# Kernel tuning notes

Measured on AMD Instinct MI355X. Metric: run time of the kernel, lower is better.

The kernel has to match this reference:

```python
import jax, jax.numpy as jnp
import numpy as np
import math

B, L, D = 8, 2048, 256


def setup_inputs() -> dict:
    key = jax.random.key(0)
    ks = jax.random.split(key, 8)
    return {
        "query": jax.random.normal(ks[0], (B, L, D), dtype=jnp.float32),
        "key": jax.random.normal(ks[1], (B, L, D), dtype=jnp.float32),
        "value": jax.random.normal(ks[2], (B, L, D), dtype=jnp.float32),
        "mask": jax.random.randint(ks[3], (B, L), 0, 2, dtype=jnp.int32),
        "Wq_w": jax.random.normal(ks[4], (D, D), dtype=jnp.float32) * 0.05,
        "Wq_b": jax.random.normal(ks[5], (D,), dtype=jnp.float32) * 0.05,
        "Wk_w": jax.random.normal(ks[6], (D, D), dtype=jnp.float32) * 0.05,
        "Wk_b": jax.random.normal(ks[7], (D,), dtype=jnp.float32) * 0.05,
    }


def reference(query, key, value, mask, Wq_w, Wq_b, Wk_w, Wk_b):
    d = query.shape[-1]
    q = query @ Wq_w.T + Wq_b            # [B, Lq, D]
    k = key @ Wk_w.T + Wk_b              # [B, Lk, D]
    scores = jnp.einsum("bqd,bkd->bqk", q, k) / math.sqrt(d)  # [B, Lq, Lk]
    m = mask.astype(scores.dtype)[:, None, :]                  # [B, 1, Lk]
    # multiplicative then additive masking, as in original
    scores = jnp.where(m == 0, jnp.asarray(-1e9, scores.dtype), scores * m)
    attn = jax.nn.softmax(scores, axis=-1)
    return jnp.einsum("bqk,bkd->bqd", attn, value)
```

## Files before the change

kernel.cpp:

```cpp
#include <hip/hip_runtime.h>
#include <stdint.h>
#include <stddef.h>

#define B_ 8
#define L_ 2048
#define D_ 256
#define KSPLIT 4
#define KRANGE 512
#define KTILE 32
#define NITER 16

typedef __bf16 bf16x8 __attribute__((ext_vector_type(8)));
typedef float floatx4 __attribute__((ext_vector_type(4)));
typedef float floatx16 __attribute__((ext_vector_type(16)));
typedef _Float16 half4_t __attribute__((ext_vector_type(4)));

__device__ __forceinline__ short f2bf(float f) {
    union { float f; uint32_t u; } v; v.f = f;
    return (short)((v.u + 0x8000u) >> 16);
}

__device__ __forceinline__ uint32_t pack2bf(float a, float b) {
    union { float f; uint32_t u; } x, y; x.f = a; y.f = b;
    return ((x.u + 0x8000u) >> 16) | ((y.u + 0x8000u) & 0xFFFF0000u);
}

__device__ __forceinline__ uint32_t cvtpk_bf16(float lo, float hi2) {
    uint32_t w;
    asm("v_cvt_pk_bf16_f32 %0, %1, %2" : "=v"(w) : "v"(lo), "v"(hi2));
    return w;
}

__device__ __forceinline__ void pl32swap(uint32_t &a, uint32_t &b) {
    asm("v_permlane32_swap_b32 %0, %1" : "+v"(a), "+v"(b));
}

__device__ __forceinline__ void async16(const void* g, void* l) {
    __builtin_amdgcn_global_load_lds(
        (__attribute__((address_space(1))) void*)g,
        (__attribute__((address_space(3))) void*)l,
        16, 0, 0);
}

__global__ __launch_bounds__(256, 3) void proj_kernel(
    const float* __restrict__ Xq, const float* __restrict__ Xk,
    const float* __restrict__ Wq, const float* __restrict__ Wk,
    const float* __restrict__ bq, const float* __restrict__ bk,
    short* __restrict__ Oq, short* __restrict__ Ok)
{
    const float* X    = blockIdx.y ? Xk : Xq;
    const float* W    = blockIdx.y ? Wk : Wq;
    const float* bias = blockIdx.y ? bk : bq;
    short* Out        = blockIdx.y ? Ok : Oq;

    __shared__ uint32_t As[2][64 * 20];
    __shared__ uint32_t Ws[2][256 * 20];

    const int tid  = threadIdx.x;
    const int wid  = tid >> 6;
    const int lane = tid & 63;
    const int m16  = lane & 15;
    const int quad = lane >> 4;
    const int row0 = blockIdx.x * 64;
    const int ar = tid >> 2, cg = tid & 3;

    floatx4 acc[16];
    const floatx4 z4 = {0.f, 0.f, 0.f, 0.f};
#pragma unroll
    for (int i = 0; i < 16; i++) acc[i] = z4;

    {
        const float* srcA = X + (size_t)(row0 + ar) * D_ + cg * 8;
        float4 a = *(const float4*)srcA, b2 = *(const float4*)(srcA + 4);
        uint4 u; u.x = pack2bf(a.x, a.y); u.y = pack2bf(a.z, a.w);
        u.z = pack2bf(b2.x, b2.y); u.w = pack2bf(b2.z, b2.w);
        *(uint4*)&As[0][ar * 20 + cg * 4] = u;
#pragma unroll
        for (int p = 0; p < 4; p++) {
            const float* srcW = W + (size_t)(p * 64 + ar) * D_ + cg * 8;
            float4 wa = *(const float4*)srcW, wb = *(const float4*)(srcW + 4);
            uint4 w; w.x = pack2bf(wa.x, wa.y); w.y = pack2bf(wa.z, wa.w);
            w.z = pack2bf(wb.x, wb.y); w.w = pack2bf(wb.z, wb.w);
            *(uint4*)&Ws[0][(p * 64 + ar) * 20 + cg * 4] = w;
        }
    }
    __syncthreads();

    for (int kc = 0; kc < 8; kc++) {
        const int buf = kc & 1;
        float4 na, nb, nwa[4], nwb[4];
        if (kc < 7) {
            const int k1 = (kc + 1) * 32;
            const float* srcA = X + (size_t)(row0 + ar) * D_ + k1 + cg * 8;
            na = *(const float4*)srcA; nb = *(const float4*)(srcA + 4);
#pragma unroll
            for (int p = 0; p < 4; p++) {
                const float* srcW = W + (size_t)(p * 64 + ar) * D_ + k1 + cg * 8;
                nwa[p] = *(const float4*)srcW; nwb[p] = *(const float4*)(srcW + 4);
            }
        }
        bf16x8 af = *(const bf16x8*)&As[buf][(wid * 16 + m16) * 20 + quad * 4];
#pragma unroll
        for (int n = 0; n < 16; n++) {
            bf16x8 bfr = *(const bf16x8*)&Ws[buf][(n * 16 + m16) * 20 + quad * 4];
            acc[n] = __builtin_amdgcn_mfma_f32_16x16x32_bf16(af, bfr, acc[n], 0, 0, 0);
        }
        if (kc < 7) {
            uint4 u; u.x = pack2bf(na.x, na.y); u.y = pack2bf(na.z, na.w);
            u.z = pack2bf(nb.x, nb.y); u.w = pack2bf(nb.z, nb.w);
            *(uint4*)&As[buf ^ 1][ar * 20 + cg * 4] = u;
#pragma unroll
            for (int p = 0; p < 4; p++) {
                uint4 w; w.x = pack2bf(nwa[p].x, nwa[p].y); w.y = pack2bf(nwa[p].z, nwa[p].w);
                w.z = pack2bf(nwb[p].x, nwb[p].y); w.w = pack2bf(nwb[p].z, nwb[p].w);
                *(uint4*)&Ws[buf ^ 1][(p * 64 + ar) * 20 + cg * 4] = w;
            }
        }
        __syncthreads();
    }
#pragma unroll
    for (int n = 0; n < 16; n++) {
        const int col = n * 16 + m16;
        const float bv = bias[col];
#pragma unroll
        for (int r = 0; r < 4; r++) {
            const int row = row0 + wid * 16 + quad * 4 + r;
            Out[(size_t)row * D_ + col] = f2bf(acc[n][r] + bv);
        }
    }
}

__global__ __launch_bounds__(256, 2) void vtrans_kernel(
    const float* __restrict__ V, short* __restrict__ Vt)
{
    __shared__ uint32_t T[256 * 20];
    const int tid = threadIdx.x;
    const int b  = blockIdx.y;
    const int l0 = blockIdx.x * 32;
    const int r2 = tid >> 4;
    const int dg = tid & 15;
    const int lp = r2 ^ ((dg & 3) << 2);
#pragma unroll
    for (int p = 0; p < 4; p++) {
        int d0 = (dg + p * 16) * 4;
        const float* src = V + ((size_t)b * L_ + l0 + r2 * 2) * D_ + d0;
        float4 e0 = *(const float4*)src;
        float4 e1 = *(const float4*)(src + D_);
        T[(d0 + 0) * 20 + lp] = pack2bf(e0.x, e1.x);
        T[(d0 + 1) * 20 + lp] = pack2bf(e0.y, e1.y);
        T[(d0 + 2) * 20 + lp] = pack2bf(e0.z, e1.z);
        T[(d0 + 3) * 20 + lp] = pack2bf(e0.w, e1.w);
    }
    __syncthreads();
#pragma unroll
    for (int p = 0; p < 4; p++) {
        int d = (tid >> 2) + p * 64;
        int c = tid & 3;
        int cp = c ^ ((d >> 2) & 3);
        uint4 u = *(const uint4*)&T[d * 20 + cp * 4];
        *(uint4*)(Vt + ((size_t)b * D_ + d) * L_ + l0 + c * 8) = u;
    }
}

__global__ __launch_bounds__(256, 2) void flash_kernel(
    const short* __restrict__ Qb, const short* __restrict__ Kb,
    const short* __restrict__ Vt, const int* __restrict__ mask,
    float* __restrict__ Out, _Float16* __restrict__ Part,
    float* __restrict__ Lpart)
{
    __shared__ short Ks[2][KTILE * 256];
    __shared__ short Vs[2][256 * KTILE];

    const int tid  = threadIdx.x;
    const int wid  = tid >> 6;
    const int lane = tid & 63;
    const int l31  = lane & 31;
    const int hi   = lane >> 5;
    const int b  = blockIdx.x;
    const int q0 = blockIdx.y * 128;
    const int z  = blockIdx.z;

    const short* kbase = Kb + ((size_t)b * L_ + z * KRANGE) * D_;
    const short* vbase = Vt + (size_t)b * D_ * L_;
    const int*   mg    = mask + b * L_ + z * KRANGE;

    bf16x8 qf[16];
    {
        const short* qrow = Qb + ((size_t)b * L_ + q0 + wid * 32 + l31) * D_ + hi * 8;
#pragma unroll
        for (int dt = 0; dt < 16; dt++)
            qf[dt] = *(const bf16x8*)(qrow + dt * 16);
    }

    floatx16 o[8];
#pragma unroll
    for (int n = 0; n < 8; n++)
#pragma unroll
        for (int r = 0; r < 16; r++) o[n][r] = 0.f;
    float rsum = 0.f;

    auto stageK = [&](int t, int bufi) {
        short* kl = &Ks[bufi][0];
#pragma unroll
        for (int c = 0; c < 4; c++) {
            int unit = wid * 4 + c;
            int row = unit * 2 + (lane >> 5);
            int g = (lane & 31) ^ (row & 7);
            async16(kbase + (size_t)(t * KTILE + row) * D_ + g * 8, kl + unit * 512);
        }
    };
    auto stageV = [&](int t, int bufi) {
        short* vl = &Vs[bufi][0];
#pragma unroll
        for (int c = 0; c < 4; c++) {
            int unit = wid * 4 + c;
            int d = unit * 16 + (lane >> 2);
            int g = (lane & 3) ^ ((lane >> 2) & 3);
            async16(vbase + (size_t)d * L_ + z * KRANGE + t * KTILE + g * 8, vl + unit * 512);
        }
    };

    stageK(0, 0);
    __builtin_amdgcn_s_waitcnt(0x0F70);
    __syncthreads();

    const float C2 = 0.09016844f;
    bf16x8 pfA, pfB;

    for (int t = 0; t < NITER; t++) {
        const int buf = t & 1;
        if (t + 1 < NITER) stageK(t + 1, buf ^ 1);
        stageV(t, buf);
        const short* kl = &Ks[buf][0];

        int mv = mg[t * KTILE + l31];

        floatx16 s;
#pragma unroll
        for (int r = 0; r < 16; r++) s[r] = 0.f;
        __builtin_amdgcn_s_setprio(1);
#pragma unroll
        for (int dt = 0; dt < 16; dt++) {
            int g = (dt * 2 + hi) ^ (l31 & 7);
            bf16x8 kf = *(const bf16x8*)(kl + l31 * 256 + g * 8);
            s = __builtin_amdgcn_mfma_f32_32x32x16_bf16(kf, qf[dt], s, 0, 0, 0);
        }
        __builtin_amdgcn_s_setprio(0);

        if (t > 0) {
            const short* vl = &Vs[buf ^ 1][0];
            __builtin_amdgcn_s_setprio(1);
#pragma unroll
            for (int n = 0; n < 8; n++) {
                int d = n * 32 + l31;
#pragma unroll
                for (int kh = 0; kh < 2; kh++) {
                    int g2 = (kh * 2 + hi) ^ (l31 & 3);
                    bf16x8 vf = *(const bf16x8*)(vl + d * 32 + g2 * 8);
                    o[n] = __builtin_amdgcn_mfma_f32_32x32x16_bf16(kh ? pfB : pfA, vf, o[n], 0, 0, 0);
                }
            }
            __builtin_amdgcn_s_setprio(0);
        }

        uint32_t mb = (uint32_t)__ballot(mv != 0) >> (hi * 4);
        uint32_t w[8];
#pragma unroll
        for (int i = 0; i < 8; i++) {
            const int r0 = 2 * i, r1 = 2 * i + 1;
            const int k0 = (r0 & 3) + 8 * (r0 >> 2);
            float e0 = ((mb >> k0) & 1) ? exp2f(s[r0] * C2) : 0.f;
            float e1 = ((mb >> (k0 + 1)) & 1) ? exp2f(s[r1] * C2) : 0.f;
            rsum += e0 + e1;
            w[i] = cvtpk_bf16(e0, e1);
        }
        pl32swap(w[0], w[2]); pl32swap(w[1], w[3]);
        pl32swap(w[4], w[6]); pl32swap(w[5], w[7]);
        {
            union { uint32_t u[4]; bf16x8 v; } ua, ub;
            ua.u[0] = w[0]; ua.u[1] = w[1]; ua.u[2] = w[2]; ua.u[3] = w[3];
            ub.u[0] = w[4]; ub.u[1] = w[5]; ub.u[2] = w[6]; ub.u[3] = w[7];
            pfA = ua.v; pfB = ub.v;
        }

        __builtin_amdgcn_s_waitcnt(0x0F70);
        __syncthreads();
    }

    {
        const short* vl = &Vs[(NITER - 1) & 1][0];
        __builtin_amdgcn_s_setprio(1);
#pragma unroll
        for (int n = 0; n < 8; n++) {
            int d = n * 32 + l31;
#pragma unroll
            for (int kh = 0; kh < 2; kh++) {
                int g2 = (kh * 2 + hi) ^ (l31 & 3);
                bf16x8 vf = *(const bf16x8*)(vl + d * 32 + g2 * 8);
                o[n] = __builtin_amdgcn_mfma_f32_32x32x16_bf16(kh ? pfB : pfA, vf, o[n], 0, 0, 0);
            }
        }
        __builtin_amdgcn_s_setprio(0);
    }

    rsum += __shfl_xor(rsum, 32);

    const size_t BLD = (size_t)B_ * L_ * D_;
    const size_t rowbase = (size_t)b * L_ + q0 + wid * 32;
    if (z == 0) {
        float* po = Out + rowbase * D_;
#pragma unroll
        for (int n = 0; n < 8; n++)
#pragma unroll
            for (int r = 0; r < 16; r++) {
                int q = (r & 3) + 8 * (r >> 2) + 4 * hi;
                po[(size_t)q * D_ + n * 32 + l31] = o[n][r];
            }
    } else {
        _Float16* pp = Part + (size_t)(z - 1) * BLD + rowbase * D_;
#pragma unroll
        for (int n = 0; n < 8; n++)
#pragma unroll
            for (int r = 0; r < 16; r++) {
                int q = (r & 3) + 8 * (r >> 2) + 4 * hi;
                pp[(size_t)q * D_ + n * 32 + l31] = (_Float16)o[n][r];
            }
    }
    if (lane < 32) {
        Lpart[(size_t)z * (B_ * L_) + rowbase + lane] = rsum;
    }
}

__global__ __launch_bounds__(256) void norm_kernel(
    float* __restrict__ Out, const _Float16* __restrict__ Part,
    const float* __restrict__ Lpart)
{
    const int idx = blockIdx.x * 256 + threadIdx.x;
    const int row = idx >> 6;
    const int c   = (idx & 63) * 4;
    const size_t off = (size_t)row * D_ + c;
    const size_t BLD = (size_t)B_ * L_ * D_;
    float4 acc = *(float4*)(Out + off);
#pragma unroll
    for (int zz = 0; zz < 3; zz++) {
        half4_t h = *(const half4_t*)(Part + zz * BLD + off);
        acc.x += (float)h.x; acc.y += (float)h.y;
        acc.z += (float)h.z; acc.w += (float)h.w;
    }
    const int BL = B_ * L_;
    float l = Lpart[row] + Lpart[BL + row] + Lpart[2 * BL + row] + Lpart[3 * BL + row];
    float inv = 1.0f / l;
    acc.x *= inv; acc.y *= inv; acc.z *= inv; acc.w *= inv;
    *(float4*)(Out + off) = acc;
}

extern "C" void kernel_launch(void* const* d_in, const int* in_sizes, int n_in,
                              void* d_out, int out_size, void* d_ws, size_t ws_size,
                              hipStream_t stream) {
    const float* query = (const float*)d_in[0];
    const float* key   = (const float*)d_in[1];
    const float* value = (const float*)d_in[2];
    const int*   mask  = (const int*)d_in[3];
    const float* Wq_w  = (const float*)d_in[4];
    const float* Wq_b  = (const float*)d_in[5];
    const float* Wk_w  = (const float*)d_in[6];
    const float* Wk_b  = (const float*)d_in[7];
    float* out = (float*)d_out;

    const size_t BLD = (size_t)B_ * L_ * D_;
    short* qb = (short*)d_ws;
    short* kb = qb + BLD;
    short* vt = kb + BLD;
    _Float16* part = (_Float16*)(vt + BLD);
    float* lpart = (float*)(part + 3 * BLD);

    proj_kernel<<<dim3(256, 2), 256, 0, stream>>>(query, key, Wq_w, Wk_w, Wq_b, Wk_b, qb, kb);
    vtrans_kernel<<<dim3(64, 8), 256, 0, stream>>>(value, vt);
    flash_kernel<<<dim3(8, 16, 4), 256, 0, stream>>>(qb, kb, vt, mask, out, part, lpart);
    norm_kernel<<<dim3((B_ * L_ * D_ / 4) / 256), 256, 0, stream>>>(out, part, lpart);
}
```

Baseline: 185.7 us.

## Re-swizzle LDS layouts, prefetch mask bits, split QK accumulators, restructure V staging

```diff
diff --git a/kernel.cpp b/kernel.cpp
--- a/kernel.cpp
+++ b/kernel.cpp
@@ -9,6 +9,8 @@
 #define KRANGE 512
 #define KTILE 32
 #define NITER 16
+
+#define WAITVM(n) __builtin_amdgcn_s_waitcnt(0x0F70 | (n))
 
 typedef __bf16 bf16x8 __attribute__((ext_vector_type(8)));
 typedef float floatx4 __attribute__((ext_vector_type(4)));
@@ -192,6 +194,11 @@
             qf[dt] = *(const bf16x8*)(qrow + dt * 16);
     }
 
+    uint32_t mbits = 0;
+#pragma unroll
+    for (int t = 0; t < NITER; t++)
+        mbits |= (mg[t * KTILE + l31] != 0 ? 1u : 0u) << t;
+
     floatx16 o[8];
 #pragma unroll
     for (int n = 0; n < 8; n++)
@@ -204,8 +211,8 @@
 #pragma unroll
         for (int c = 0; c < 4; c++) {
             int unit = wid * 4 + c;
-            int row = unit * 2 + (lane >> 5);
-            int g = (lane & 31) ^ (row & 7);
+            int row = unit * 2 + hi;
+            int g = l31 ^ (row & 7) ^ ((row >> 3) & 3);
             async16(kbase + (size_t)(t * KTILE + row) * D_ + g * 8, kl + unit * 512);
         }
     };
@@ -215,14 +222,15 @@
         for (int c = 0; c < 4; c++) {
             int unit = wid * 4 + c;
             int d = unit * 16 + (lane >> 2);
-            int g = (lane & 3) ^ ((lane >> 2) & 3);
+            int g = (lane & 3) ^ ((lane >> 3) & 3) ^ ((lane >> 5) & 1);
             async16(vbase + (size_t)d * L_ + z * KRANGE + t * KTILE + g * 8, vl + unit * 512);
         }
     };
 
     stageK(0, 0);
-    __builtin_amdgcn_s_waitcnt(0x0F70);
-    __syncthreads();
+    stageV(0, 0);
+    WAITVM(4);
+    __builtin_amdgcn_s_barrier();
 
     const float C2 = 0.09016844f;
     bf16x8 pfA, pfB;
@@ -230,20 +238,20 @@
     for (int t = 0; t < NITER; t++) {
         const int buf = t & 1;
         if (t + 1 < NITER) stageK(t + 1, buf ^ 1);
-        stageV(t, buf);
         const short* kl = &Ks[buf][0];
 
-        int mv = mg[t * KTILE + l31];
-
-        floatx16 s;
-#pragma unroll
-        for (int r = 0; r < 16; r++) s[r] = 0.f;
+        floatx16 s0, s1;
+#pragma unroll
+        for (int r = 0; r < 16; r++) { s0[r] = 0.f; s1[r] = 0.f; }
         __builtin_amdgcn_s_setprio(1);
 #pragma unroll
-        for (int dt = 0; dt < 16; dt++) {
-            int g = (dt * 2 + hi) ^ (l31 & 7);
-            bf16x8 kf = *(const bf16x8*)(kl + l31 * 256 + g * 8);
-            s = __builtin_amdgcn_mfma_f32_32x32x16_bf16(kf, qf[dt], s, 0, 0, 0);
+        for (int dt = 0; dt < 16; dt += 2) {
+            int g0 = (dt * 2 + hi) ^ (l31 & 7) ^ ((l31 >> 3) & 3);
+            int g1 = ((dt + 1) * 2 + hi) ^ (l31 & 7) ^ ((l31 >> 3) & 3);
+            bf16x8 kf0 = *(const bf16x8*)(kl + l31 * 256 + g0 * 8);
+            bf16x8 kf1 = *(const bf16x8*)(kl + l31 * 256 + g1 * 8);
+            s0 = __builtin_amdgcn_mfma_f32_32x32x16_bf16(kf0, qf[dt], s0, 0, 0, 0);
+            s1 = __builtin_amdgcn_mfma_f32_32x32x16_bf16(kf1, qf[dt + 1], s1, 0, 0, 0);
         }
         __builtin_amdgcn_s_setprio(0);
 
@@ -255,7 +263,7 @@
                 int d = n * 32 + l31;
 #pragma unroll
                 for (int kh = 0; kh < 2; kh++) {
-                    int g2 = (kh * 2 + hi) ^ (l31 & 3);
+                    int g2 = (kh * 2 + hi) ^ ((l31 >> 1) & 3) ^ ((l31 >> 3) & 1);
                     bf16x8 vf = *(const bf16x8*)(vl + d * 32 + g2 * 8);
                     o[n] = __builtin_amdgcn_mfma_f32_32x32x16_bf16(kh ? pfB : pfA, vf, o[n], 0, 0, 0);
                 }
@@ -263,14 +271,21 @@
             __builtin_amdgcn_s_setprio(0);
         }
 
-        uint32_t mb = (uint32_t)__ballot(mv != 0) >> (hi * 4);
+        if (t + 1 < NITER) {
+            __builtin_amdgcn_s_barrier();
+            stageV(t + 1, buf ^ 1);
+        }
+
+        uint32_t mb = (uint32_t)__ballot((mbits >> t) & 1) >> (hi * 4);
         uint32_t w[8];
 #pragma unroll
         for (int i = 0; i < 8; i++) {
             const int r0 = 2 * i, r1 = 2 * i + 1;
             const int k0 = (r0 & 3) + 8 * (r0 >> 2);
-            float e0 = ((mb >> k0) & 1) ? exp2f(s[r0] * C2) : 0.f;
-            float e1 = ((mb >> (k0 + 1)) & 1) ? exp2f(s[r1] * C2) : 0.f;
+            float sv0 = s0[r0] + s1[r0];
+            float sv1 = s0[r1] + s1[r1];
+            float e0 = ((mb >> k0) & 1) ? exp2f(sv0 * C2) : 0.f;
+            float e1 = ((mb >> (k0 + 1)) & 1) ? exp2f(sv1 * C2) : 0.f;
             rsum += e0 + e1;
             w[i] = cvtpk_bf16(e0, e1);
         }
@@ -283,8 +298,8 @@
             pfA = ua.v; pfB = ub.v;
         }
 
-        __builtin_amdgcn_s_waitcnt(0x0F70);
-        __syncthreads();
+        if (t + 1 < NITER) WAITVM(4); else WAITVM(0);
+        __builtin_amdgcn_s_barrier();
     }
 
     {
@@ -295,7 +310,7 @@
             int d = n * 32 + l31;
 #pragma unroll
             for (int kh = 0; kh < 2; kh++) {
-                int g2 = (kh * 2 + hi) ^ (l31 & 3);
+                int g2 = (kh * 2 + hi) ^ ((l31 >> 1) & 3) ^ ((l31 >> 3) & 1);
                 bf16x8 vf = *(const bf16x8*)(vl + d * 32 + g2 * 8);
                 o[n] = __builtin_amdgcn_mfma_f32_32x32x16_bf16(kh ? pfB : pfA, vf, o[n], 0, 0, 0);
             }
```

Measured after the change: 189.9 us. +2.3%, slower.
